# Kernel tuning notes

Hardware: AMD Instinct MI355X
Metric: run time of the kernel (lower is better)

The kernel has to match this reference:

```python
import jax, jax.numpy as jnp
import numpy as np

N_DIM = 256
NHIDDEN = 256
NLAYERS = 4
LAMDA = 0.5
ALPHA = 0.1
MODAL_WEIGHT = 1.0
N_SPEAKERS = 2
B_DIA = 100   # number of dialogues
L_DIA = 40    # utterances per dialogue
N_UTT = B_DIA * L_DIA


def _cos_sim_blocks(x, B, L):
    # per-dialogue cosine-similarity blocks: x [N, d] -> [B, L, L]
    xb = x.reshape(B, L, -1)
    xn = xb / jnp.linalg.norm(xb, axis=-1, keepdims=True)
    cos = jnp.einsum('bid,bjd->bij', xn, xn) * 0.99999
    return 1.0 - jnp.arccos(cos) / jnp.pi


def setup_inputs() -> dict:
    key = jax.random.key(0)
    ks = jax.random.split(key, 8)
    return {
        'a': jax.random.normal(ks[0], (N_UTT, N_DIM), jnp.float32),
        'v': jax.random.normal(ks[1], (N_UTT, N_DIM), jnp.float32),
        'l': jax.random.normal(ks[2], (N_UTT, N_DIM), jnp.float32),
        'qmask': jax.random.uniform(ks[3], (L_DIA, B_DIA, N_SPEAKERS), jnp.float32),
        'spk_emb': jax.random.normal(ks[4], (N_SPEAKERS, N_DIM), jnp.float32) * 0.02,
        'W0': jax.random.normal(ks[5], (N_DIM, NHIDDEN), jnp.float32) / np.sqrt(N_DIM).astype(np.float32),
        'b0': jnp.zeros((NHIDDEN,), jnp.float32),
        'Wconvs': jax.random.normal(ks[6], (NLAYERS, NHIDDEN, NHIDDEN), jnp.float32) / np.sqrt(NHIDDEN).astype(np.float32),
        'dia_len_each': L_DIA,
        'n_dialogues': B_DIA,
    }


def reference(a, v, l, qmask, spk_emb, W0, b0, Wconvs, dia_len_each, n_dialogues):
    B, L = n_dialogues, dia_len_each
    N = B * L
    M = 3  # modals 'avl'

    # --- speaker embedding added to text modality (use_speaker) ---
    # torch.cat([qmask[:x, i, :] for i, x in enumerate(dia_len)]) with equal lengths
    q = jnp.transpose(qmask, (1, 0, 2)).reshape(N, -1)   # [N, n_speakers]
    spk_idx = jnp.argmax(q, axis=-1)                      # [N]
    l = l + spk_emb[spk_idx]

    feats = [a, v, l]
    normed = [f / jnp.linalg.norm(f, axis=-1, keepdims=True) for f in feats]

    # --- create_big_adj: block-diag per-modal cosine-sim blocks + cross-modal diagonals ---
    adj = jnp.zeros((M * N, M * N), jnp.float32)
    idx = jnp.arange(N).reshape(B, L)
    rows = idx[:, :, None]   # [B, L, 1]
    cols = idx[:, None, :]   # [B, 1, L]
    ar = jnp.arange(N)
    for m in range(M):
        sim = _cos_sim_blocks(feats[m], B, L)            # [B, L, L]
        adj = adj.at[m * N + rows, m * N + cols].set(sim)
    for m in range(M):
        for n in range(M):
            if m == n:
                continue
            cs = jnp.sum(normed[m] * normed[n], axis=-1) * 0.99999
            dia_sim = 1.0 - jnp.arccos(cs) / jnp.pi
            adj = adj.at[m * N + ar, n * N + ar].set(dia_sim * MODAL_WEIGHT)
    d = jnp.sum(adj, axis=1)
    dinv = d ** -0.5
    adj = adj * dinv[:, None] * dinv[None, :]            # D^-1/2 A D^-1/2

    # --- GCNII_lyc propagation (eval mode, variant=False, no dropout) ---
    x = jnp.concatenate(feats, axis=0)                   # [3N, n_dim]
    h0 = jax.nn.relu(x @ W0 + b0)
    h = h0
    for i in range(NLAYERS):
        theta = float(np.log(LAMDA / (i + 1) + 1.0))
        hi = adj @ h
        support = (1.0 - ALPHA) * hi + ALPHA * h0
        h = jax.nn.relu(theta * (support @ Wconvs[i]) + (1.0 - theta) * support)
    feat = jnp.concatenate([x, h], axis=-1)              # use_residue

    # regroup modalities per utterance: [N, 3*(n_dim+nhidden)]
    out = jnp.concatenate([feat[:N], feat[N:2 * N], feat[2 * N:3 * N]], axis=-1)
    return out
```

## Files before the change

kernel.cpp:

```cpp
#include <hip/hip_runtime.h>
#include <hip/hip_bf16.h>

#define N_UTT 4000
#define NDIM 256
#define B_DIA 100
#define L_DIA 40
#define NLAYERS 4

typedef __attribute__((ext_vector_type(8))) short short8;
typedef __attribute__((ext_vector_type(4))) float f32x4;

union bfpk4 { __hip_bfloat16 h[4]; uint2 u; };

static __device__ __forceinline__ float bf2f(__hip_bfloat16 h) {
  union { float f; unsigned u; } x;
  x.u = ((unsigned)*(unsigned short*)&h) << 16;
  return x.f;
}

__global__ void k_wt(const float* __restrict__ W0, const float* __restrict__ Wc,
                     __hip_bfloat16* __restrict__ Wt) {
  int k0 = blockIdx.x * 64, n0 = blockIdx.y * 64, g = blockIdx.z;
  int t = threadIdx.x;
  const float* src = (g == 0) ? W0 : (Wc + (g - 1) * NDIM * NDIM);
  __shared__ float tile[64][65];
  #pragma unroll
  for (int it = 0; it < 16; it++) {
    int e = t + 256 * it;
    int row = e >> 6, col = e & 63;
    tile[row][col] = src[(k0 + row) * NDIM + n0 + col];
  }
  __syncthreads();
  #pragma unroll
  for (int it = 0; it < 16; it++) {
    int e = t + 256 * it;
    int row = e >> 6, col = e & 63;
    Wt[(g * NDIM + n0 + row) * NDIM + k0 + col] = __float2bfloat16(tile[col][row]);
  }
}

__global__ __launch_bounds__(512, 1) void k_main(
    const float* __restrict__ a, const float* __restrict__ v,
    const float* __restrict__ lf, const float* __restrict__ qmask,
    const float* __restrict__ spk, const float* __restrict__ b0,
    const __hip_bfloat16* __restrict__ Wt, float* __restrict__ out) {
  __shared__ __hip_bfloat16 xls[3][L_DIA][264];
  __shared__ __hip_bfloat16 hls[3][NDIM][L_DIA];
  __shared__ __hip_bfloat16 sext[3][L_DIA][136];
  __shared__ float invn[120];
  __shared__ float dinv[120];
  __shared__ float psum[120][4];

  int b = blockIdx.x;
  int t = threadIdx.x;
  int w = t >> 6, ln = t & 63;
  int l15 = ln & 15, lk = (ln >> 4) * 8;
  const float inv_pi = 0.31830988618379067f;

  int arows[3], cols[2];
  #pragma unroll
  for (int rt = 0; rt < 3; rt++) {
    int rr_ = rt * 16 + l15;
    arows[rt] = (rr_ < L_DIA) ? rr_ : (L_DIA - 1);
  }
  #pragma unroll
  for (int c = 0; c < 2; c++) cols[c] = w * 32 + c * 16 + l15;

  {
    unsigned int* sz = (unsigned int*)&sext[0][0][0];
    #pragma unroll
    for (int e = t; e < 3 * L_DIA * 136 / 2; e += 512) sz[e] = 0u;
  }
  for (int e = t; e < 120 * 64; e += 512) {
    int r = e >> 6, c4 = e & 63;
    int m = r / L_DIA, p = r - m * L_DIA;
    int i = b * L_DIA + p;
    float4 val;
    if (m == 0)      val = ((const float4*)a)[i * 64 + c4];
    else if (m == 1) val = ((const float4*)v)[i * 64 + c4];
    else {
      val = ((const float4*)lf)[i * 64 + c4];
      float q0 = qmask[(p * B_DIA + b) * 2 + 0];
      float q1 = qmask[(p * B_DIA + b) * 2 + 1];
      int s = (q1 > q0) ? 1 : 0;
      float4 sv = ((const float4*)spk)[s * 64 + c4];
      val.x += sv.x; val.y += sv.y; val.z += sv.z; val.w += sv.w;
    }
    ((float4*)out)[i * 384 + m * 128 + c4] = val;
    bfpk4 pk;
    pk.h[0] = __float2bfloat16(val.x); pk.h[1] = __float2bfloat16(val.y);
    pk.h[2] = __float2bfloat16(val.z); pk.h[3] = __float2bfloat16(val.w);
    *(uint2*)&xls[m][p][c4 * 4] = pk.u;
  }
  __syncthreads();

  if (t < 480) {
    int r = t >> 2, q4 = t & 3;
    int m = r / L_DIA, p = r - m * L_DIA;
    float s = 0.f;
    #pragma unroll
    for (int jj = 0; jj < 8; jj++) {
      short8 vv = *(const short8*)&xls[m][p][q4 * 64 + jj * 8];
      #pragma unroll
      for (int e = 0; e < 8; e++) {
        union { float f; unsigned u; } x;
        x.u = ((unsigned)(unsigned short)vv[e]) << 16;
        s += x.f * x.f;
      }
    }
    psum[r][q4] = s;
  }
  __syncthreads();
  if (t < 120) invn[t] = rsqrtf(psum[t][0] + psum[t][1] + psum[t][2] + psum[t][3]);
  __syncthreads();

  if (w < 3) {
    int mA = w;
    f32x4 sacc[3][3];
    #pragma unroll
    for (int rt = 0; rt < 3; rt++)
      #pragma unroll
      for (int ct = 0; ct < 3; ct++) sacc[rt][ct] = (f32x4){0.f,0.f,0.f,0.f};
    #pragma unroll
    for (int k0 = 0; k0 < NDIM; k0 += 32) {
      short8 fr[3];
      #pragma unroll
      for (int rt = 0; rt < 3; rt++)
        fr[rt] = *(const short8*)&xls[mA][arows[rt]][k0 + lk];
      #pragma unroll
      for (int rt = 0; rt < 3; rt++)
        #pragma unroll
        for (int ct = 0; ct < 3; ct++)
          sacc[rt][ct] = __builtin_amdgcn_mfma_f32_16x16x32_bf16(fr[rt], fr[ct], sacc[rt][ct], 0, 0, 0);
    }
    #pragma unroll
    for (int rt = 0; rt < 3; rt++)
      #pragma unroll
      for (int ct = 0; ct < 3; ct++)
        #pragma unroll
        for (int rr = 0; rr < 4; rr++) {
          int row = rt * 16 + (ln >> 4) * 4 + rr;
          int col = ct * 16 + l15;
          if (row < L_DIA && col < L_DIA) {
            float cs = sacc[rt][ct][rr] * invn[mA * 40 + row] * invn[mA * 40 + col] * 0.99999f;
            cs = fminf(fmaxf(cs, -1.f), 1.f);
            sext[mA][row][col] = __float2bfloat16(1.f - acosf(cs) * inv_pi);
          }
        }
  } else if (w < 6) {
    int pi = w - 3;
    int mA = (pi == 2) ? 1 : 0, mB = (pi == 0) ? 1 : 2;
    int slotA = (pi == 0) ? 40 : 80, slotB = (pi == 2) ? 80 : 40;
    f32x4 dacc[3];
    #pragma unroll
    for (int rt = 0; rt < 3; rt++) dacc[rt] = (f32x4){0.f,0.f,0.f,0.f};
    #pragma unroll
    for (int k0 = 0; k0 < NDIM; k0 += 32) {
      short8 frA[3], frB[3];
      #pragma unroll
      for (int rt = 0; rt < 3; rt++) {
        frA[rt] = *(const short8*)&xls[mA][arows[rt]][k0 + lk];
        frB[rt] = *(const short8*)&xls[mB][arows[rt]][k0 + lk];
      }
      #pragma unroll
      for (int rt = 0; rt < 3; rt++)
        dacc[rt] = __builtin_amdgcn_mfma_f32_16x16x32_bf16(frA[rt], frB[rt], dacc[rt], 0, 0, 0);
    }
    #pragma unroll
    for (int rt = 0; rt < 3; rt++)
      #pragma unroll
      for (int rr = 0; rr < 4; rr++) {
        int row = rt * 16 + (ln >> 4) * 4 + rr;
        if (l15 == ((ln >> 4) * 4 + rr) && row < L_DIA) {
          float cs = dacc[rt][rr] * invn[mA * 40 + row] * invn[mB * 40 + row] * 0.99999f;
          cs = fminf(fmaxf(cs, -1.f), 1.f);
          __hip_bfloat16 vv = __float2bfloat16(1.f - acosf(cs) * inv_pi);
          sext[mA][row][slotA + row] = vv;
          sext[mB][row][slotB + row] = vv;
        }
      }
  }
  __syncthreads();

  if (t < 120) {
    int m = t / 40, p = t - m * 40;
    float d = 0.f;
    #pragma unroll 10
    for (int q = 0; q < 40; q++) d += bf2f(sext[m][p][q]);
    d += bf2f(sext[m][p][40 + p]) + bf2f(sext[m][p][80 + p]);
    dinv[t] = rsqrtf(d);
  }
  __syncthreads();
  for (int e = t; e < 5040; e += 512) {
    if (e < 4800) {
      int m = e / 1600, rem = e - m * 1600;
      int p = rem / 40, q = rem - p * 40;
      sext[m][p][q] = __float2bfloat16(
          bf2f(sext[m][p][q]) * 0.9f * dinv[m * 40 + p] * dinv[m * 40 + q]);
    } else {
      int idx = e - 4800;
      int m = idx / 80, j = idx - m * 80;
      int which = j / 40, p = j - which * 40;
      int pmx = which ? ((m == 2) ? 1 : 2) : ((m == 0) ? 1 : 0);
      int k = 40 * (1 + which) + p;
      sext[m][p][k] = __float2bfloat16(
          bf2f(sext[m][p][k]) * 0.9f * dinv[m * 40 + p] * dinv[pmx * 40 + p]);
    }
  }
  __syncthreads();

  uint2 h0r[9][2];
  {
    f32x4 acc[9][2];
    #pragma unroll
    for (int s = 0; s < 9; s++)
      #pragma unroll
      for (int c = 0; c < 2; c++) acc[s][c] = (f32x4){0.f,0.f,0.f,0.f};
    #pragma unroll
    for (int k0 = 0; k0 < NDIM; k0 += 32) {
      short8 bfw[2];
      #pragma unroll
      for (int c = 0; c < 2; c++)
        bfw[c] = *(const short8*)&Wt[cols[c] * NDIM + k0 + lk];
      short8 af[9];
      #pragma unroll
      for (int s = 0; s < 9; s++)
        af[s] = *(const short8*)&xls[s / 3][arows[s % 3]][k0 + lk];
      #pragma unroll
      for (int s = 0; s < 9; s++)
        #pragma unroll
        for (int c = 0; c < 2; c++)
          acc[s][c] = __builtin_amdgcn_mfma_f32_16x16x32_bf16(af[s], bfw[c], acc[s][c], 0, 0, 0);
    }
    #pragma unroll
    for (int s = 0; s < 9; s++) {
      int p0 = (s % 3) * 16 + (ln >> 4) * 4;
      #pragma unroll
      for (int c = 0; c < 2; c++) {
        float bias = b0[cols[c]];
        bfpk4 pk;
        #pragma unroll
        for (int rr = 0; rr < 4; rr++)
          pk.h[rr] = __float2bfloat16(fmaxf(acc[s][c][rr] + bias, 0.f));
        h0r[s][c] = pk.u;
        if (p0 < L_DIA) *(uint2*)&hls[s / 3][cols[c]][p0] = pk.u;
      }
    }
  }
  __syncthreads();

  const float thetas[NLAYERS] = {0.40546510810816438f, 0.22314355131420976f,
                                 0.15415067982725836f, 0.11778303565638346f};
  #pragma unroll
  for (int li = 0; li < NLAYERS; li++) {
    float th = thetas[li], onemt = 1.f - th;
    const __hip_bfloat16* Wl = Wt + (li + 1) * NDIM * NDIM;

    {
      f32x4 acc[9][2];
      #pragma unroll
      for (int s = 0; s < 9; s++)
        #pragma unroll
        for (int c = 0; c < 2; c++) acc[s][c] = (f32x4){0.f,0.f,0.f,0.f};
      #pragma unroll
      for (int j = 0; j < 4; j++) {
        int kk = j * 32 + lk;
        short8 bfv[3][2];
        #pragma unroll
        for (int mm = 0; mm < 3; mm++) {
          int pm0 = (mm == 0) ? 1 : 0, pm1 = (mm == 2) ? 1 : 2;
          int srcm, brow;
          if (kk < 40)       { srcm = mm;  brow = kk; }
          else if (kk < 80)  { srcm = pm0; brow = kk - 40; }
          else if (kk < 120) { srcm = pm1; brow = kk - 80; }
          else               { srcm = pm1; brow = 32; }
          #pragma unroll
          for (int c = 0; c < 2; c++)
            bfv[mm][c] = *(const short8*)&hls[srcm][cols[c]][brow];
        }
        short8 af[9];
        #pragma unroll
        for (int s = 0; s < 9; s++)
          af[s] = *(const short8*)&sext[s / 3][arows[s % 3]][j * 32 + lk];
        #pragma unroll
        for (int s = 0; s < 9; s++)
          #pragma unroll
          for (int c = 0; c < 2; c++)
            acc[s][c] = __builtin_amdgcn_mfma_f32_16x16x32_bf16(af[s], bfv[s / 3][c], acc[s][c], 0, 0, 0);
      }
      #pragma unroll
      for (int s = 0; s < 9; s++) {
        int m = s / 3;
        int p0 = (s % 3) * 16 + (ln >> 4) * 4;
        #pragma unroll
        for (int c = 0; c < 2; c++) {
          bfpk4 h0p; h0p.u = h0r[s][c];
          if (p0 < L_DIA) {
            #pragma unroll
            for (int rr = 0; rr < 4; rr++)
              xls[m][p0 + rr][cols[c]] =
                  __float2bfloat16(acc[s][c][rr] + 0.1f * bf2f(h0p.h[rr]));
          }
        }
      }
    }
    __syncthreads();

    {
      f32x4 o[9][2];
      #pragma unroll
      for (int s = 0; s < 9; s++)
        #pragma unroll
        for (int c = 0; c < 2; c++) o[s][c] = (f32x4){0.f,0.f,0.f,0.f};
      #pragma unroll
      for (int k0 = 0; k0 < NDIM; k0 += 32) {
        short8 bfw[2];
        #pragma unroll
        for (int c = 0; c < 2; c++)
          bfw[c] = *(const short8*)&Wl[cols[c] * NDIM + k0 + lk];
        short8 af[9];
        #pragma unroll
        for (int s = 0; s < 9; s++)
          af[s] = *(const short8*)&xls[s / 3][arows[s % 3]][k0 + lk];
        #pragma unroll
        for (int s = 0; s < 9; s++)
          #pragma unroll
          for (int c = 0; c < 2; c++)
            o[s][c] = __builtin_amdgcn_mfma_f32_16x16x32_bf16(af[s], bfw[c], o[s][c], 0, 0, 0);
      }
      #pragma unroll
      for (int s = 0; s < 9; s++) {
        int m = s / 3;
        int p0 = (s % 3) * 16 + (ln >> 4) * 4;
        if (p0 >= L_DIA) continue;
        #pragma unroll
        for (int c = 0; c < 2; c++) {
          int col = cols[c];
          if (li < NLAYERS - 1) {
            bfpk4 pk;
            #pragma unroll
            for (int rr = 0; rr < 4; rr++) {
              float supv = bf2f(xls[m][p0 + rr][col]);
              pk.h[rr] = __float2bfloat16(fmaxf(th * o[s][c][rr] + onemt * supv, 0.f));
            }
            *(uint2*)&hls[m][col][p0] = pk.u;
          } else {
            #pragma unroll
            for (int rr = 0; rr < 4; rr++) {
              float supv = bf2f(xls[m][p0 + rr][col]);
              out[(b * L_DIA + p0 + rr) * 1536 + m * 512 + 256 + col] =
                  fmaxf(th * o[s][c][rr] + onemt * supv, 0.f);
            }
          }
        }
      }
    }
    __syncthreads();
  }
}

extern "C" void kernel_launch(void* const* d_in, const int* in_sizes, int n_in,
                              void* d_out, int out_size, void* d_ws, size_t ws_size,
                              hipStream_t stream) {
  const float* a     = (const float*)d_in[0];
  const float* v     = (const float*)d_in[1];
  const float* lf    = (const float*)d_in[2];
  const float* qmask = (const float*)d_in[3];
  const float* spk   = (const float*)d_in[4];
  const float* W0    = (const float*)d_in[5];
  const float* b0    = (const float*)d_in[6];
  const float* Wc    = (const float*)d_in[7];
  float* out = (float*)d_out;

  __hip_bfloat16* Wt = (__hip_bfloat16*)d_ws;

  k_wt<<<dim3(4, 4, 5), 256, 0, stream>>>(W0, Wc, Wt);
  k_main<<<B_DIA, 512, 0, stream>>>(a, v, lf, qmask, spk, b0, Wt, out);
}
```

Measured before the change: 63.34 us.

## Halve block to 256 threads with four column tiles per wave

Reduces the per-dialogue block from 8 waves to 4 waves. Each wave now covers 64 output columns (four 16-wide tiles) instead of 32, and the cross-modal diagonal work is looped in the waves that previously had idle peers. This doubles per-wave accumulator registers (9x4 f32x4 tiles plus h0 cache) and halves parallelism per block. Only 100 blocks run on a large GPU, so latency hiding drops while per-wave reuse of loaded A fragments increases.

```diff
diff --git a/kernel.cpp b/kernel.cpp
--- a/kernel.cpp
+++ b/kernel.cpp
@@ -6,6 +6,7 @@
 #define B_DIA 100
 #define L_DIA 40
 #define NLAYERS 4
+#define NT 256
 
 typedef __attribute__((ext_vector_type(8))) short short8;
 typedef __attribute__((ext_vector_type(4))) float f32x4;
@@ -39,7 +40,7 @@
   }
 }
 
-__global__ __launch_bounds__(512, 1) void k_main(
+__global__ __launch_bounds__(NT, 1) void k_main(
     const float* __restrict__ a, const float* __restrict__ v,
     const float* __restrict__ lf, const float* __restrict__ qmask,
     const float* __restrict__ spk, const float* __restrict__ b0,
@@ -55,23 +56,23 @@
   int t = threadIdx.x;
   int w = t >> 6, ln = t & 63;
   int l15 = ln & 15, lk = (ln >> 4) * 8;
+  int hi4 = (ln >> 4) * 4;
   const float inv_pi = 0.31830988618379067f;
 
-  int arows[3], cols[2];
+  int arows[3], cols[4];
   #pragma unroll
   for (int rt = 0; rt < 3; rt++) {
     int rr_ = rt * 16 + l15;
     arows[rt] = (rr_ < L_DIA) ? rr_ : (L_DIA - 1);
   }
   #pragma unroll
-  for (int c = 0; c < 2; c++) cols[c] = w * 32 + c * 16 + l15;
+  for (int c = 0; c < 4; c++) cols[c] = w * 64 + c * 16 + l15;
 
   {
     unsigned int* sz = (unsigned int*)&sext[0][0][0];
-    #pragma unroll
-    for (int e = t; e < 3 * L_DIA * 136 / 2; e += 512) sz[e] = 0u;
-  }
-  for (int e = t; e < 120 * 64; e += 512) {
+    for (int e = t; e < 3 * L_DIA * 136 / 2; e += NT) sz[e] = 0u;
+  }
+  for (int e = t; e < 120 * 64; e += NT) {
     int r = e >> 6, c4 = e & 63;
     int m = r / L_DIA, p = r - m * L_DIA;
     int i = b * L_DIA + p;
@@ -94,8 +95,8 @@
   }
   __syncthreads();
 
-  if (t < 480) {
-    int r = t >> 2, q4 = t & 3;
+  for (int it = t; it < 480; it += NT) {
+    int r = it >> 2, q4 = it & 3;
     int m = r / L_DIA, p = r - m * L_DIA;
     float s = 0.f;
     #pragma unroll
@@ -139,7 +140,7 @@
       for (int ct = 0; ct < 3; ct++)
         #pragma unroll
         for (int rr = 0; rr < 4; rr++) {
-          int row = rt * 16 + (ln >> 4) * 4 + rr;
+          int row = rt * 16 + hi4 + rr;
           int col = ct * 16 + l15;
           if (row < L_DIA && col < L_DIA) {
             float cs = sacc[rt][ct][rr] * invn[mA * 40 + row] * invn[mA * 40 + col] * 0.99999f;
@@ -147,38 +148,40 @@
             sext[mA][row][col] = __float2bfloat16(1.f - acosf(cs) * inv_pi);
           }
         }
-  } else if (w < 6) {
-    int pi = w - 3;
-    int mA = (pi == 2) ? 1 : 0, mB = (pi == 0) ? 1 : 2;
-    int slotA = (pi == 0) ? 40 : 80, slotB = (pi == 2) ? 80 : 40;
-    f32x4 dacc[3];
-    #pragma unroll
-    for (int rt = 0; rt < 3; rt++) dacc[rt] = (f32x4){0.f,0.f,0.f,0.f};
-    #pragma unroll
-    for (int k0 = 0; k0 < NDIM; k0 += 32) {
-      short8 frA[3], frB[3];
-      #pragma unroll
-      for (int rt = 0; rt < 3; rt++) {
-        frA[rt] = *(const short8*)&xls[mA][arows[rt]][k0 + lk];
-        frB[rt] = *(const short8*)&xls[mB][arows[rt]][k0 + lk];
+  } else {
+    #pragma unroll
+    for (int pi = 0; pi < 3; pi++) {
+      int mA = (pi == 2) ? 1 : 0, mB = (pi == 0) ? 1 : 2;
+      int slotA = (pi == 0) ? 40 : 80, slotB = (pi == 2) ? 80 : 40;
+      f32x4 dacc[3];
+      #pragma unroll
+      for (int rt = 0; rt < 3; rt++) dacc[rt] = (f32x4){0.f,0.f,0.f,0.f};
+      #pragma unroll
+      for (int k0 = 0; k0 < NDIM; k0 += 32) {
+        short8 frA[3], frB[3];
+        #pragma unroll
+        for (int rt = 0; rt < 3; rt++) {
+          frA[rt] = *(const short8*)&xls[mA][arows[rt]][k0 + lk];
+          frB[rt] = *(const short8*)&xls[mB][arows[rt]][k0 + lk];
+        }
+        #pragma unroll
+        for (int rt = 0; rt < 3; rt++)
+          dacc[rt] = __builtin_amdgcn_mfma_f32_16x16x32_bf16(frA[rt], frB[rt], dacc[rt], 0, 0, 0);
       }
       #pragma unroll
       for (int rt = 0; rt < 3; rt++)
-        dacc[rt] = __builtin_amdgcn_mfma_f32_16x16x32_bf16(frA[rt], frB[rt], dacc[rt], 0, 0, 0);
-    }
-    #pragma unroll
-    for (int rt = 0; rt < 3; rt++)
-      #pragma unroll
-      for (int rr = 0; rr < 4; rr++) {
-        int row = rt * 16 + (ln >> 4) * 4 + rr;
-        if (l15 == ((ln >> 4) * 4 + rr) && row < L_DIA) {
-          float cs = dacc[rt][rr] * invn[mA * 40 + row] * invn[mB * 40 + row] * 0.99999f;
-          cs = fminf(fmaxf(cs, -1.f), 1.f);
-          __hip_bfloat16 vv = __float2bfloat16(1.f - acosf(cs) * inv_pi);
-          sext[mA][row][slotA + row] = vv;
-          sext[mB][row][slotB + row] = vv;
-        }
-      }
+        #pragma unroll
+        for (int rr = 0; rr < 4; rr++) {
+          int row = rt * 16 + hi4 + rr;
+          if (l15 == (hi4 + rr) && row < L_DIA) {
+            float cs = dacc[rt][rr] * invn[mA * 40 + row] * invn[mB * 40 + row] * 0.99999f;
+            cs = fminf(fmaxf(cs, -1.f), 1.f);
+            __hip_bfloat16 vv = __float2bfloat16(1.f - acosf(cs) * inv_pi);
+            sext[mA][row][slotA + row] = vv;
+            sext[mB][row][slotB + row] = vv;
+          }
+        }
+    }
   }
   __syncthreads();
 
@@ -191,7 +194,7 @@
     dinv[t] = rsqrtf(d);
   }
   __syncthreads();
-  for (int e = t; e < 5040; e += 512) {
+  for (int e = t; e < 5040; e += NT) {
     if (e < 4800) {
       int m = e / 1600, rem = e - m * 1600;
       int p = rem / 40, q = rem - p * 40;
@@ -209,18 +212,18 @@
   }
   __syncthreads();
 
-  uint2 h0r[9][2];
+  uint2 h0r[9][4];
   {
-    f32x4 acc[9][2];
+    f32x4 acc[9][4];
     #pragma unroll
     for (int s = 0; s < 9; s++)
       #pragma unroll
-      for (int c = 0; c < 2; c++) acc[s][c] = (f32x4){0.f,0.f,0.f,0.f};
+      for (int c = 0; c < 4; c++) acc[s][c] = (f32x4){0.f,0.f,0.f,0.f};
     #pragma unroll
     for (int k0 = 0; k0 < NDIM; k0 += 32) {
-      short8 bfw[2];
-      #pragma unroll
-      for (int c = 0; c < 2; c++)
+      short8 bfw[4];
+      #pragma unroll
+      for (int c = 0; c < 4; c++)
         bfw[c] = *(const short8*)&Wt[cols[c] * NDIM + k0 + lk];
       short8 af[9];
       #pragma unroll
@@ -229,14 +232,14 @@
       #pragma unroll
       for (int s = 0; s < 9; s++)
         #pragma unroll
-        for (int c = 0; c < 2; c++)
+        for (int c = 0; c < 4; c++)
           acc[s][c] = __builtin_amdgcn_mfma_f32_16x16x32_bf16(af[s], bfw[c], acc[s][c], 0, 0, 0);
     }
     #pragma unroll
     for (int s = 0; s < 9; s++) {
-      int p0 = (s % 3) * 16 + (ln >> 4) * 4;
-      #pragma unroll
-      for (int c = 0; c < 2; c++) {
+      int p0 = (s % 3) * 16 + hi4;
+      #pragma unroll
+      for (int c = 0; c < 4; c++) {
         float bias = b0[cols[c]];
         bfpk4 pk;
         #pragma unroll
@@ -257,15 +260,15 @@
     const __hip_bfloat16* Wl = Wt + (li + 1) * NDIM * NDIM;
 
     {
-      f32x4 acc[9][2];
+      f32x4 acc[9][4];
       #pragma unroll
       for (int s = 0; s < 9; s++)
         #pragma unroll
-        for (int c = 0; c < 2; c++) acc[s][c] = (f32x4){0.f,0.f,0.f,0.f};
+        for (int c = 0; c < 4; c++) acc[s][c] = (f32x4){0.f,0.f,0.f,0.f};
       #pragma unroll
       for (int j = 0; j < 4; j++) {
         int kk = j * 32 + lk;
-        short8 bfv[3][2];
+        short8 bfv[3][4];
         #pragma unroll
         for (int mm = 0; mm < 3; mm++) {
           int pm0 = (mm == 0) ? 1 : 0, pm1 = (mm == 2) ? 1 : 2;
@@ -275,7 +278,7 @@
           else if (kk < 120) { srcm = pm1; brow = kk - 80; }
           else               { srcm = pm1; brow = 32; }
           #pragma unroll
-          for (int c = 0; c < 2; c++)
+          for (int c = 0; c < 4; c++)
             bfv[mm][c] = *(const short8*)&hls[srcm][cols[c]][brow];
         }
         short8 af[9];
@@ -285,15 +288,15 @@
         #pragma unroll
         for (int s = 0; s < 9; s++)
           #pragma unroll
-          for (int c = 0; c < 2; c++)
+          for (int c = 0; c < 4; c++)
             acc[s][c] = __builtin_amdgcn_mfma_f32_16x16x32_bf16(af[s], bfv[s / 3][c], acc[s][c], 0, 0, 0);
       }
       #pragma unroll
       for (int s = 0; s < 9; s++) {
         int m = s / 3;
-        int p0 = (s % 3) * 16 + (ln >> 4) * 4;
-        #pragma unroll
-        for (int c = 0; c < 2; c++) {
+        int p0 = (s % 3) * 16 + hi4;
+        #pragma unroll
+        for (int c = 0; c < 4; c++) {
           bfpk4 h0p; h0p.u = h0r[s][c];
           if (p0 < L_DIA) {
             #pragma unroll
@@ -307,16 +310,16 @@
     __syncthreads();
 
     {
-      f32x4 o[9][2];
+      f32x4 o[9][4];
       #pragma unroll
       for (int s = 0; s < 9; s++)
         #pragma unroll
-        for (int c = 0; c < 2; c++) o[s][c] = (f32x4){0.f,0.f,0.f,0.f};
+        for (int c = 0; c < 4; c++) o[s][c] = (f32x4){0.f,0.f,0.f,0.f};
       #pragma unroll
       for (int k0 = 0; k0 < NDIM; k0 += 32) {
-        short8 bfw[2];
-        #pragma unroll
-        for (int c = 0; c < 2; c++)
+        short8 bfw[4];
+        #pragma unroll
+        for (int c = 0; c < 4; c++)
           bfw[c] = *(const short8*)&Wl[cols[c] * NDIM + k0 + lk];
         short8 af[9];
         #pragma unroll
@@ -325,16 +328,16 @@
         #pragma unroll
         for (int s = 0; s < 9; s++)
           #pragma unroll
-          for (int c = 0; c < 2; c++)
+          for (int c = 0; c < 4; c++)
             o[s][c] = __builtin_amdgcn_mfma_f32_16x16x32_bf16(af[s], bfw[c], o[s][c], 0, 0, 0);
       }
       #pragma unroll
       for (int s = 0; s < 9; s++) {
         int m = s / 3;
-        int p0 = (s % 3) * 16 + (ln >> 4) * 4;
+        int p0 = (s % 3) * 16 + hi4;
         if (p0 >= L_DIA) continue;
         #pragma unroll
-        for (int c = 0; c < 2; c++) {
+        for (int c = 0; c < 4; c++) {
           int col = cols[c];
           if (li < NLAYERS - 1) {
             bfpk4 pk;
@@ -375,5 +378,5 @@
   __hip_bfloat16* Wt = (__hip_bfloat16*)d_ws;
 
   k_wt<<<dim3(4, 4, 5), 256, 0, stream>>>(W0, Wc, Wt);
-  k_main<<<B_DIA, 512, 0, stream>>>(a, v, lf, qmask, spk, b0, Wt, out);
+  k_main<<<B_DIA, NT, 0, stream>>>(a, v, lf, qmask, spk, b0, Wt, out);
 }
```

New measurement: 87.12 us. 1.38x slower.
